# Kernel tuning notes

Hardware: AMD Instinct MI355X
Metric: run time of the kernel (lower is better)

The kernel has to match this reference:

```python
import jax, jax.numpy as jnp
import numpy as np

N = 4096
D = 256
H = 8
HD = D // H
EPS = 1e-5
NEG = -1e9


def layer_norm(x, g, b):
    mu = jnp.mean(x, axis=-1, keepdims=True)
    var = jnp.mean(jnp.square(x - mu), axis=-1, keepdims=True)
    return (x - mu) * jax.lax.rsqrt(var + EPS) * g + b


def setup_inputs() -> dict:
    key = jax.random.key(0)
    ks = jax.random.split(key, 12)
    s = 1.0 / np.sqrt(D)
    inp = {
        "x": jax.random.normal(ks[0], (N, D), dtype=jnp.float32),
        "adj": jax.random.randint(ks[1], (N, N), 0, 2, dtype=jnp.int32),
        "Wq": jax.random.uniform(ks[2], (D, D), jnp.float32, -s, s),
        "Wk": jax.random.uniform(ks[3], (D, D), jnp.float32, -s, s),
        "Wv": jax.random.uniform(ks[4], (D, D), jnp.float32, -s, s),
        "bq": jnp.zeros((D,), jnp.float32),
        "bk": jnp.zeros((D,), jnp.float32),
        "bv": jnp.zeros((D,), jnp.float32),
        "Wo": jax.random.uniform(ks[5], (D, D), jnp.float32, -s, s),
        "bo": jnp.zeros((D,), jnp.float32),
        "g1": jnp.ones((D,), jnp.float32),
        "beta1": jnp.zeros((D,), jnp.float32),
        "W1": jax.random.uniform(ks[6], (2 * D, D), jnp.float32, -s, s),
        "b1": jnp.zeros((2 * D,), jnp.float32),
        "W2": jax.random.uniform(ks[7], (D, 2 * D), jnp.float32, -1.0 / np.sqrt(2 * D), 1.0 / np.sqrt(2 * D)),
        "b2": jnp.zeros((D,), jnp.float32),
        "g2": jnp.ones((D,), jnp.float32),
        "beta2": jnp.zeros((D,), jnp.float32),
    }
    return inp


def reference(x, adj, Wq, Wk, Wv, bq, bk, bv, Wo, bo, g1, beta1, W1, b1, W2, b2, g2, beta2):
    n = adj.shape[0]
    # allowed = adj + I > 0 ; attention only over neighbors + self-loop
    allowed = (adj + jnp.eye(n, dtype=adj.dtype)) > 0  # (n, n) bool

    q = (x @ Wq.T + bq).reshape(n, H, HD)
    k = (x @ Wk.T + bk).reshape(n, H, HD)
    v = (x @ Wv.T + bv).reshape(n, H, HD)

    scale = 1.0 / np.sqrt(HD)
    scores = jnp.einsum('nhd,mhd->hnm', q, k) * scale  # (H, n, n)
    scores = jnp.where(allowed[None, :, :], scores, NEG)
    attn = jax.nn.softmax(scores, axis=-1)
    o = jnp.einsum('hnm,mhd->nhd', attn, v).reshape(n, D)
    h = o @ Wo.T + bo

    x = layer_norm(x + h, g1, beta1)
    ffn = jax.nn.relu(x @ W1.T + b1) @ W2.T + b2
    x = layer_norm(x + ffn, g2, beta2)
    return x
```

## Files before the change

### kernel.cpp

```cpp
#include <hip/hip_runtime.h>
#include <hip/hip_bf16.h>

typedef __attribute__((ext_vector_type(4))) float f32x4;
typedef __attribute__((ext_vector_type(8))) short s16x8;

#define NROWS 4096
#define DMODEL 256
#define NHEAD 8
#define HDIM 32
#define PSTRIDE 72
#define OSTRIDE 33
#define M2C 24.0f
#define NM (NROWS * DMODEL)
#define SH_S 268
#define SY_S 264
#define SR_S 520

__device__ __forceinline__ short bf16r(float f) {
    union { float f; unsigned u; } v; v.f = f;
    unsigned r = v.u + 0x7fffu + ((v.u >> 16) & 1u);
    return (short)(r >> 16);
}

__device__ __forceinline__ float fexp2(float x) {
    float r;
    asm("v_exp_f32 %0, %1" : "=v"(r) : "v"(x));
    return r;
}

__device__ __forceinline__ unsigned pk_bf16(float a, float b) {
#if __has_builtin(__builtin_amdgcn_cvt_pk_bf16_f32)
    typedef __bf16 bf2 __attribute__((ext_vector_type(2)));
    union { bf2 h; unsigned u; } c;
    c.h = __builtin_amdgcn_cvt_pk_bf16_f32(a, b);
    return c.u;
#else
    return (unsigned)(unsigned short)bf16r(a) | ((unsigned)(unsigned short)bf16r(b) << 16);
#endif
}

__device__ __forceinline__ s16x8 pack8(float4 a, float4 b) {
    s16x8 r;
    r[0] = bf16r(a.x); r[1] = bf16r(a.y); r[2] = bf16r(a.z); r[3] = bf16r(a.w);
    r[4] = bf16r(b.x); r[5] = bf16r(b.y); r[6] = bf16r(b.z); r[7] = bf16r(b.w);
    return r;
}

__global__ __launch_bounds__(256) void prep1_kernel(
        const int* __restrict__ adj, unsigned* __restrict__ mask,
        const float* __restrict__ Wo, const float* __restrict__ W1,
        const float* __restrict__ W2, short* __restrict__ Wb,
        const float* __restrict__ Wq, const float* __restrict__ Wk,
        const float* __restrict__ Wv, short* __restrict__ Wqkvb,
        const float* __restrict__ X, short* __restrict__ Xb) {
    const int b = blockIdx.x;
    const int tid = threadIdx.x;
    const int lane = tid & 63;
    if (b < 2048) {
        const int waveid = b * 4 + (tid >> 6);
        int4 av[8];
        int rows[8], segs[8];
#pragma unroll
        for (int i = 0; i < 8; ++i) {
            const int task = waveid + i * 8192;
            rows[i] = task >> 4; segs[i] = task & 15;
            av[i] = *(const int4*)(adj + (size_t)rows[i] * NROWS + segs[i] * 256 + lane * 4);
        }
#pragma unroll
        for (int i = 0; i < 8; ++i) {
            const int row = rows[i];
            const int c0 = segs[i] * 256 + lane * 4;
            unsigned nib = (unsigned)(av[i].x > 0 || c0 == row)
                         | ((unsigned)(av[i].y > 0 || c0 + 1 == row) << 1)
                         | ((unsigned)(av[i].z > 0 || c0 + 2 == row) << 2)
                         | ((unsigned)(av[i].w > 0 || c0 + 3 == row) << 3);
            unsigned v = nib << ((lane & 7) * 4);
            v |= __shfl_xor((int)v, 1, 64);
            v |= __shfl_xor((int)v, 2, 64);
            v |= __shfl_xor((int)v, 4, 64);
            if ((lane & 7) == 0)
                mask[row * 128 + segs[i] * 8 + (lane >> 3)] = v;
        }
    } else if (b < 2208) {
        int i = (b - 2048) * 2048 + tid * 8;
        const float* src; int off;
        if (i < 65536)       { src = Wo; off = i; }
        else if (i < 196608) { src = W1; off = i - 65536; }
        else                 { src = W2; off = i - 196608; }
        *(s16x8*)(Wb + i) = pack8(*(const float4*)(src + off), *(const float4*)(src + off + 4));
    } else if (b < 2304) {
        int i = (b - 2208) * 2048 + tid * 8;
        const float* src; int off;
        if (i < 65536)       { src = Wq; off = i; }
        else if (i < 131072) { src = Wk; off = i - 65536; }
        else                 { src = Wv; off = i - 131072; }
        *(s16x8*)(Wqkvb + i) = pack8(*(const float4*)(src + off), *(const float4*)(src + off + 4));
    } else {
        int i = (b - 2304) * 2048 + tid * 8;
        *(s16x8*)(Xb + i) = pack8(*(const float4*)(X + i), *(const float4*)(X + i + 4));
    }
}

__global__ __launch_bounds__(256) void prep2_kernel(
        const short* __restrict__ Xb, const short* __restrict__ Wqkvb,
        const float* __restrict__ bq, const float* __restrict__ bk,
        const float* __restrict__ bv,
        short* __restrict__ Qb, short* __restrict__ Kb,
        short* __restrict__ Vswz) {
    __shared__ short sT[64 * 72];
    const int b = blockIdx.x;
    const int tid = threadIdx.x;
    const int lane = tid & 63;
    const int wv = tid >> 6;
    const int quad = lane >> 4, col = lane & 15;
    const int bx = b & 63, by = b >> 6;
    const int o0 = by * 64;
    const int z = o0 >> 8;
    const float* bias = (z == 0) ? bq : (z == 1 ? bk : bv);
    const int ow0 = o0 & 255;
    const int n0 = bx * 64 + wv * 16;
    const float QSC = 0.25505653437397888f;

    f32x4 zero = {0.f, 0.f, 0.f, 0.f};
    f32x4 acc[4] = {zero, zero, zero, zero};
    const short* ap = Xb + (size_t)(n0 + col) * DMODEL + quad * 8;
#pragma unroll
    for (int k0 = 0; k0 < DMODEL; k0 += 32) {
        s16x8 af = *(const s16x8*)(ap + k0);
#pragma unroll
        for (int t = 0; t < 4; ++t) {
            s16x8 bf = *(const s16x8*)(Wqkvb + (size_t)(o0 + t * 16 + col) * DMODEL + quad * 8 + k0);
            acc[t] = __builtin_amdgcn_mfma_f32_16x16x32_bf16(af, bf, acc[t], 0, 0, 0);
        }
    }
    if (z != 2) {
#pragma unroll
        for (int t = 0; t < 4; ++t) {
            const int oo = ow0 + t * 16 + col;
            float bvv = bias[oo];
#pragma unroll
            for (int r = 0; r < 4; ++r) {
                int n = n0 + quad * 4 + r;
                float v = acc[t][r] + bvv;
                if (z == 0) Qb[(size_t)n * DMODEL + oo] = bf16r(v * QSC);
                else        Kb[(size_t)(oo >> 5) * NROWS * HDIM + (size_t)n * HDIM + (oo & 31)] = bf16r(v);
            }
        }
    } else {
#pragma unroll
        for (int t = 0; t < 4; ++t) {
            const int oot = t * 16 + col;
            float bvv = bias[ow0 + oot];
#pragma unroll
            for (int r = 0; r < 4; ++r) {
                int nn = wv * 16 + quad * 4 + r;
                sT[oot * 72 + nn] = bf16r(acc[t][r] + bvv);
            }
        }
        __syncthreads();
        const int f = tid >> 5;
        const int lh = f >> 2, hdh = (f >> 1) & 1, kh = f & 1;
        const int L0 = (tid & 31) * 2;
        const int hgl = (ow0 >> 5) + lh;
        short* dst = Vswz + (((size_t)(hgl * 64 + bx) * 4 + hdh * 2 + kh) * 512);
#pragma unroll
        for (int e = 0; e < 2; ++e) {
            int L = L0 + e;
            int hd_local = lh * 32 + hdh * 16 + (L & 15);
            int key_local = kh * 32 + ((L >> 4) * 8);
            s16x8 v = *(const s16x8*)&sT[hd_local * 72 + key_local];
            *(s16x8*)(dst + L * 8) = v;
        }
    }
}

__global__ __launch_bounds__(256) void attn_kernel(const short* __restrict__ Qb,
                                                   const short* __restrict__ Kb,
                                                   const short* __restrict__ Vswz,
                                                   const unsigned* __restrict__ mask,
                                                   short* __restrict__ Om) {
    __shared__ union {
        short sP[2][16 * PSTRIDE];
        float sO[HDIM][OSTRIDE];
    } u[4];
    __shared__ float sl[4][32];
    __shared__ __align__(16) unsigned lut2[32];

    const int tid = threadIdx.x;
    const int wv = tid >> 6, lane = tid & 63;
    const int quad = lane >> 4, col = lane & 15;
    const int h = blockIdx.x & 7;
    const int q0 = (blockIdx.x >> 3) * 32;
    const int kw = wv * 1024;

    if (tid < 32) {
        int i = tid >> 1;
        unsigned b0 = (tid & 1) ? ((i >> 2) & 1u) : (i & 1u);
        unsigned b1 = (tid & 1) ? ((i >> 3) & 1u) : ((i >> 1) & 1u);
        lut2[tid] = (b0 ? 0xFFFFu : 0u) | (b1 ? 0xFFFF0000u : 0u);
    }
    __syncthreads();

    s16x8 qf[2];
    qf[0] = *(const s16x8*)(Qb + (size_t)(q0 + col) * DMODEL + h * HDIM + quad * 8);
    qf[1] = *(const s16x8*)(Qb + (size_t)(q0 + 16 + col) * DMODEL + h * HDIM + quad * 8);

    const short* kp = Kb + (size_t)h * NROWS * HDIM + (size_t)(kw + col) * HDIM + quad * 8;
    const short* vbase = Vswz + ((size_t)(h * 64 + (kw >> 6)) * 4) * 512 + lane * 8;
    const unsigned* mp0 = mask + (size_t)(q0 + col) * 128 + (kw >> 5);
    const unsigned* mp1 = mp0 + 16 * 128;

    const short onev = (col == 0) ? (short)0x3F80 : (short)0;
    const s16x8 ones = {onev, onev, onev, onev, onev, onev, onev, onev};

    f32x4 zero = {0.f, 0.f, 0.f, 0.f};
    f32x4 acc[2][2] = {{zero, zero}, {zero, zero}};
    f32x4 lacc[2] = {zero, zero};
    const f32x4 cinit = {-M2C, -M2C, -M2C, -M2C};
    const int sh_lo = quad * 4, sh_hi = 16 + quad * 4;
    const char* lb = (const char*)lut2;

#pragma unroll 2
    for (int it = 0; it < 16; ++it) {
        const short* k = kp + it * 64 * HDIM;
        s16x8 kf0 = *(const s16x8*)(k);
        s16x8 kf1 = *(const s16x8*)(k + 16 * HDIM);
        s16x8 kf2 = *(const s16x8*)(k + 32 * HDIM);
        s16x8 kf3 = *(const s16x8*)(k + 48 * HDIM);
        uint2 w0 = *(const uint2*)(mp0 + it * 2);
        uint2 w1 = *(const uint2*)(mp1 + it * 2);
        const short* vb = vbase + it * 4 * 512;
        s16x8 vf00 = *(const s16x8*)(vb);
        s16x8 vf01 = *(const s16x8*)(vb + 512);
        s16x8 vf10 = *(const s16x8*)(vb + 1024);
        s16x8 vf11 = *(const s16x8*)(vb + 1536);

#pragma unroll
        for (int qs = 0; qs < 2; ++qs) {
            const unsigned wx = qs ? w1.x : w0.x;
            const unsigned wy = qs ? w1.y : w0.y;
            uint2 m0 = *(const uint2*)(lb + (((wx >> sh_lo) & 0xF) << 3));
            uint2 m1 = *(const uint2*)(lb + (((wx >> sh_hi) & 0xF) << 3));
            uint2 m2 = *(const uint2*)(lb + (((wy >> sh_lo) & 0xF) << 3));
            uint2 m3 = *(const uint2*)(lb + (((wy >> sh_hi) & 0xF) << 3));

            f32x4 st[4];
            st[0] = __builtin_amdgcn_mfma_f32_16x16x32_bf16(kf0, qf[qs], cinit, 0, 0, 0);
            st[1] = __builtin_amdgcn_mfma_f32_16x16x32_bf16(kf1, qf[qs], cinit, 0, 0, 0);
            st[2] = __builtin_amdgcn_mfma_f32_16x16x32_bf16(kf2, qf[qs], cinit, 0, 0, 0);
            st[3] = __builtin_amdgcn_mfma_f32_16x16x32_bf16(kf3, qf[qs], cinit, 0, 0, 0);

            short* pb = &u[wv].sP[qs][0];
            uint2 pr;
            pr.x = pk_bf16(fexp2(st[0][0]), fexp2(st[0][1])) & m0.x;
            pr.y = pk_bf16(fexp2(st[0][2]), fexp2(st[0][3])) & m0.y;
            *(uint2*)(pb + col * PSTRIDE + 0 * 16 + quad * 4) = pr;
            pr.x = pk_bf16(fexp2(st[1][0]), fexp2(st[1][1])) & m1.x;
            pr.y = pk_bf16(fexp2(st[1][2]), fexp2(st[1][3])) & m1.y;
            *(uint2*)(pb + col * PSTRIDE + 1 * 16 + quad * 4) = pr;
            pr.x = pk_bf16(fexp2(st[2][0]), fexp2(st[2][1])) & m2.x;
            pr.y = pk_bf16(fexp2(st[2][2]), fexp2(st[2][3])) & m2.y;
            *(uint2*)(pb + col * PSTRIDE + 2 * 16 + quad * 4) = pr;
            pr.x = pk_bf16(fexp2(st[3][0]), fexp2(st[3][1])) & m3.x;
            pr.y = pk_bf16(fexp2(st[3][2]), fexp2(st[3][3])) & m3.y;
            *(uint2*)(pb + col * PSTRIDE + 3 * 16 + quad * 4) = pr;

            s16x8 pb0 = *(const s16x8*)(pb + col * PSTRIDE + quad * 8);
            s16x8 pb1 = *(const s16x8*)(pb + col * PSTRIDE + 32 + quad * 8);

            acc[qs][0] = __builtin_amdgcn_mfma_f32_16x16x32_bf16(vf00, pb0, acc[qs][0], 0, 0, 0);
            acc[qs][0] = __builtin_amdgcn_mfma_f32_16x16x32_bf16(vf01, pb1, acc[qs][0], 0, 0, 0);
            acc[qs][1] = __builtin_amdgcn_mfma_f32_16x16x32_bf16(vf10, pb0, acc[qs][1], 0, 0, 0);
            acc[qs][1] = __builtin_amdgcn_mfma_f32_16x16x32_bf16(vf11, pb1, acc[qs][1], 0, 0, 0);
            lacc[qs] = __builtin_amdgcn_mfma_f32_16x16x32_bf16(ones, pb0, lacc[qs], 0, 0, 0);
            lacc[qs] = __builtin_amdgcn_mfma_f32_16x16x32_bf16(ones, pb1, lacc[qs], 0, 0, 0);
        }
    }

#pragma unroll
    for (int qs = 0; qs < 2; ++qs) {
        if (lane < 16) sl[wv][qs * 16 + col] = lacc[qs][0];
#pragma unroll
        for (int rr = 0; rr < 4; ++rr) {
            u[wv].sO[quad * 4 + rr][qs * 16 + col]      = acc[qs][0][rr];
            u[wv].sO[16 + quad * 4 + rr][qs * 16 + col] = acc[qs][1][rr];
        }
    }
    __syncthreads();

    const int q = tid >> 3, hd0 = (tid & 7) * 4;
    float l = sl[0][q] + sl[1][q] + sl[2][q] + sl[3][q];
    float inv = 1.f / l;
    float4 ov;
    ov.x = u[0].sO[hd0][q]     + u[1].sO[hd0][q]     + u[2].sO[hd0][q]     + u[3].sO[hd0][q];
    ov.y = u[0].sO[hd0 + 1][q] + u[1].sO[hd0 + 1][q] + u[2].sO[hd0 + 1][q] + u[3].sO[hd0 + 1][q];
    ov.z = u[0].sO[hd0 + 2][q] + u[1].sO[hd0 + 2][q] + u[2].sO[hd0 + 2][q] + u[3].sO[hd0 + 2][q];
    ov.w = u[0].sO[hd0 + 3][q] + u[1].sO[hd0 + 3][q] + u[2].sO[hd0 + 3][q] + u[3].sO[hd0 + 3][q];
    uint2 ob;
    ob.x = pk_bf16(ov.x * inv, ov.y * inv);
    ob.y = pk_bf16(ov.z * inv, ov.w * inv);
    *(uint2*)(Om + (size_t)(q0 + q) * DMODEL + h * HDIM + hd0) = ob;
}

__global__ __launch_bounds__(512) void mega_kernel(
        const short* __restrict__ Omb,
        const float* __restrict__ X,
        const short* __restrict__ Wob, const short* __restrict__ W1b,
        const short* __restrict__ W2b,
        const float* __restrict__ bo,
        const float* __restrict__ g1, const float* __restrict__ be1,
        const float* __restrict__ b1, const float* __restrict__ b2,
        const float* __restrict__ g2, const float* __restrict__ be2,
        float* __restrict__ out) {
    __shared__ short sR[16 * SR_S];
    __shared__ float sH[16 * SH_S];
    __shared__ short sY[16 * SY_S];

    const int tid = threadIdx.x;
    const int wv = tid >> 6, lane = tid & 63;
    const int quad = lane >> 4, col = lane & 15;
    const int n0 = blockIdx.x * 16;
    const int rr_ = tid >> 5, c8 = (tid & 31) * 8;
    const int n_ln = n0 + rr_;
    f32x4 zero = {0.f, 0.f, 0.f, 0.f};

    {
        const int o0 = wv * 32;
        f32x4 acc[2] = {zero, zero};
#pragma unroll
        for (int k0 = 0; k0 < DMODEL; k0 += 32) {
            s16x8 af = *(const s16x8*)(Omb + (size_t)(n0 + col) * DMODEL + k0 + quad * 8);
#pragma unroll
            for (int t = 0; t < 2; ++t) {
                s16x8 bf = *(const s16x8*)(Wob + (size_t)(o0 + t * 16 + col) * DMODEL + k0 + quad * 8);
                acc[t] = __builtin_amdgcn_mfma_f32_16x16x32_bf16(af, bf, acc[t], 0, 0, 0);
            }
        }
#pragma unroll
        for (int t = 0; t < 2; ++t) {
            int o = o0 + t * 16 + col;
            float bv = bo[o];
#pragma unroll
            for (int r = 0; r < 4; ++r)
                sH[(quad * 4 + r) * SH_S + o] = acc[t][r] + bv;
        }
    }
    __syncthreads();

    float y1v[8];
    {
        const float* xp = X + (size_t)n_ln * DMODEL + c8;
        float v[8];
        float s = 0.f;
#pragma unroll
        for (int j = 0; j < 2; ++j) {
            float4 xv = ((const float4*)xp)[j];
            float4 hv = *(const float4*)&sH[rr_ * SH_S + c8 + j * 4];
            v[j * 4 + 0] = xv.x + hv.x; v[j * 4 + 1] = xv.y + hv.y;
            v[j * 4 + 2] = xv.z + hv.z; v[j * 4 + 3] = xv.w + hv.w;
            s += v[j * 4] + v[j * 4 + 1] + v[j * 4 + 2] + v[j * 4 + 3];
        }
#pragma unroll
        for (int m = 1; m < 32; m <<= 1) s += __shfl_xor(s, m, 64);
        float mean = s * (1.f / 256.f);
        float q = 0.f;
#pragma unroll
        for (int i = 0; i < 8; ++i) { v[i] -= mean; q += v[i] * v[i]; }
#pragma unroll
        for (int m = 1; m < 32; m <<= 1) q += __shfl_xor(q, m, 64);
        float rstd = rsqrtf(q * (1.f / 256.f) + 1e-5f);
        const float* gp = g1 + c8;
        const float* bp = be1 + c8;
        s16x8 w;
#pragma unroll
        for (int j = 0; j < 2; ++j) {
            float4 gv = ((const float4*)gp)[j];
            float4 bev = ((const float4*)bp)[j];
            float a0 = v[j * 4 + 0] * rstd * gv.x + bev.x;
            float a1 = v[j * 4 + 1] * rstd * gv.y + bev.y;
            float a2 = v[j * 4 + 2] * rstd * gv.z + bev.z;
            float a3 = v[j * 4 + 3] * rstd * gv.w + bev.w;
            y1v[j * 4 + 0] = a0; y1v[j * 4 + 1] = a1;
            y1v[j * 4 + 2] = a2; y1v[j * 4 + 3] = a3;
            *((unsigned*)&w + j * 2 + 0) = pk_bf16(a0, a1);
            *((unsigned*)&w + j * 2 + 1) = pk_bf16(a2, a3);
        }
        *(s16x8*)&sY[rr_ * SY_S + c8] = w;
    }
    __syncthreads();

    {
        const int o0 = wv * 64;
        f32x4 acc[4] = {zero, zero, zero, zero};
#pragma unroll
        for (int k0 = 0; k0 < DMODEL; k0 += 32) {
            s16x8 af = *(const s16x8*)&sY[col * SY_S + k0 + quad * 8];
#pragma unroll
            for (int t = 0; t < 4; ++t) {
                s16x8 bf = *(const s16x8*)(W1b + (size_t)(o0 + t * 16 + col) * DMODEL + k0 + quad * 8);
                acc[t] = __builtin_amdgcn_mfma_f32_16x16x32_bf16(af, bf, acc[t], 0, 0, 0);
            }
        }
#pragma unroll
        for (int t = 0; t < 4; ++t) {
            int o = o0 + t * 16 + col;
            float bv = b1[o];
#pragma unroll
            for (int r = 0; r < 4; ++r)
                sR[(quad * 4 + r) * SR_S + o] = bf16r(fmaxf(acc[t][r] + bv, 0.f));
        }
    }
    __syncthreads();

    {
        const int o0 = wv * 32;
        f32x4 acc[2] = {zero, zero};
#pragma unroll
        for (int k0 = 0; k0 < 512; k0 += 32) {
            s16x8 af = *(const s16x8*)&sR[col * SR_S + k0 + quad * 8];
#pragma unroll
            for (int t = 0; t < 2; ++t) {
                s16x8 bf = *(const s16x8*)(W2b + (size_t)(o0 + t * 16 + col) * 512 + k0 + quad * 8);
                acc[t] = __builtin_amdgcn_mfma_f32_16x16x32_bf16(af, bf, acc[t], 0, 0, 0);
            }
        }
#pragma unroll
        for (int t = 0; t < 2; ++t) {
            int o = o0 + t * 16 + col;
            float bv = b2[o];
#pragma unroll
            for (int r = 0; r < 4; ++r)
                sH[(quad * 4 + r) * SH_S + o] = acc[t][r] + bv;
        }
    }
    __syncthreads();

    {
        float v[8];
        float s = 0.f;
#pragma unroll
        for (int j = 0; j < 2; ++j) {
            float4 hv = *(const float4*)&sH[rr_ * SH_S + c8 + j * 4];
            v[j * 4 + 0] = y1v[j * 4 + 0] + hv.x; v[j * 4 + 1] = y1v[j * 4 + 1] + hv.y;
            v[j * 4 + 2] = y1v[j * 4 + 2] + hv.z; v[j * 4 + 3] = y1v[j * 4 + 3] + hv.w;
            s += v[j * 4] + v[j * 4 + 1] + v[j * 4 + 2] + v[j * 4 + 3];
        }
#pragma unroll
        for (int m = 1; m < 32; m <<= 1) s += __shfl_xor(s, m, 64);
        float mean = s * (1.f / 256.f);
        float q = 0.f;
#pragma unroll
        for (int i = 0; i < 8; ++i) { v[i] -= mean; q += v[i] * v[i]; }
#pragma unroll
        for (int m = 1; m < 32; m <<= 1) q += __shfl_xor(q, m, 64);
        float rstd = rsqrtf(q * (1.f / 256.f) + 1e-5f);
        const float* gp = g2 + c8;
        const float* bp = be2 + c8;
        float* op = out + (size_t)n_ln * DMODEL + c8;
#pragma unroll
        for (int j = 0; j < 2; ++j) {
            float4 gv = ((const float4*)gp)[j];
            float4 bev = ((const float4*)bp)[j];
            float4 y;
            y.x = v[j * 4 + 0] * rstd * gv.x + bev.x;
            y.y = v[j * 4 + 1] * rstd * gv.y + bev.y;
            y.z = v[j * 4 + 2] * rstd * gv.z + bev.z;
            y.w = v[j * 4 + 3] * rstd * gv.w + bev.w;
            ((float4*)op)[j] = y;
        }
    }
}

extern "C" void kernel_launch(void* const* d_in, const int* in_sizes, int n_in,
                              void* d_out, int out_size, void* d_ws, size_t ws_size,
                              hipStream_t stream) {
    const float* x   = (const float*)d_in[0];
    const int*   adj = (const int*)d_in[1];
    const float* Wq  = (const float*)d_in[2];
    const float* Wk  = (const float*)d_in[3];
    const float* Wv  = (const float*)d_in[4];
    const float* bq  = (const float*)d_in[5];
    const float* bk  = (const float*)d_in[6];
    const float* bv  = (const float*)d_in[7];
    const float* Wo  = (const float*)d_in[8];
    const float* bo  = (const float*)d_in[9];
    const float* g1  = (const float*)d_in[10];
    const float* be1 = (const float*)d_in[11];
    const float* W1  = (const float*)d_in[12];
    const float* b1  = (const float*)d_in[13];
    const float* W2  = (const float*)d_in[14];
    const float* b2  = (const float*)d_in[15];
    const float* g2  = (const float*)d_in[16];
    const float* be2 = (const float*)d_in[17];
    float* out = (float*)d_out;

    char* p = (char*)d_ws;
    unsigned* mask = (unsigned*)p; p += (size_t)NROWS * 128 * 4;
    short* Wb    = (short*)p;      p += (size_t)327680 * 2;
    short* Wqkvb = (short*)p;      p += (size_t)196608 * 2;
    short* Xb    = (short*)p;      p += (size_t)NM * 2;
    short* Qb    = (short*)p;      p += (size_t)NM * 2;
    short* Kb    = (short*)p;      p += (size_t)NM * 2;
    short* Vswz  = (short*)p;      p += (size_t)NM * 2;
    short* Omb   = (short*)p;      p += (size_t)NM * 2;

    prep1_kernel<<<dim3(2816), dim3(256), 0, stream>>>(
        adj, mask, Wo, W1, W2, Wb, Wq, Wk, Wv, Wqkvb, x, Xb);
    prep2_kernel<<<dim3(768), dim3(256), 0, stream>>>(
        Xb, Wqkvb, bq, bk, bv, Qb, Kb, Vswz);
    attn_kernel<<<dim3(1024), dim3(256), 0, stream>>>(Qb, Kb, Vswz, mask, Omb);
    mega_kernel<<<dim3(256), dim3(512), 0, stream>>>(
        Omb, x, Wb, Wb + 65536, Wb + 196608,
        bo, g1, be1, b1, b2, g2, be2, out);
}
```

Baseline: 212.2 us.

## Keep softmax probabilities in registers by permuting the V key layout

```diff
diff --git a/kernel.cpp b/kernel.cpp
--- a/kernel.cpp
+++ b/kernel.cpp
@@ -8,7 +8,6 @@
 #define DMODEL 256
 #define NHEAD 8
 #define HDIM 32
-#define PSTRIDE 72
 #define OSTRIDE 33
 #define M2C 24.0f
 #define NM (NROWS * DMODEL)
@@ -167,9 +166,11 @@
         for (int e = 0; e < 2; ++e) {
             int L = L0 + e;
             int hd_local = lh * 32 + hdh * 16 + (L & 15);
-            int key_local = kh * 32 + ((L >> 4) * 8);
-            s16x8 v = *(const s16x8*)&sT[hd_local * 72 + key_local];
-            *(s16x8*)(dst + L * 8) = v;
+            int base = kh * 32 + (L >> 4) * 4;
+            uint2 lo = *(const uint2*)&sT[hd_local * 72 + base];
+            uint2 hi = *(const uint2*)&sT[hd_local * 72 + base + 16];
+            *(uint2*)(dst + L * 8) = lo;
+            *(uint2*)(dst + L * 8 + 4) = hi;
         }
     }
 }
@@ -179,10 +180,7 @@
                                                    const short* __restrict__ Vswz,
                                                    const unsigned* __restrict__ mask,
                                                    short* __restrict__ Om) {
-    __shared__ union {
-        short sP[2][16 * PSTRIDE];
-        float sO[HDIM][OSTRIDE];
-    } u[4];
+    __shared__ float sO[4][HDIM][OSTRIDE];
     __shared__ float sl[4][32];
     __shared__ __align__(16) unsigned lut2[32];
 
@@ -250,30 +248,22 @@
             st[2] = __builtin_amdgcn_mfma_f32_16x16x32_bf16(kf2, qf[qs], cinit, 0, 0, 0);
             st[3] = __builtin_amdgcn_mfma_f32_16x16x32_bf16(kf3, qf[qs], cinit, 0, 0, 0);
 
-            short* pb = &u[wv].sP[qs][0];
-            uint2 pr;
-            pr.x = pk_bf16(fexp2(st[0][0]), fexp2(st[0][1])) & m0.x;
-            pr.y = pk_bf16(fexp2(st[0][2]), fexp2(st[0][3])) & m0.y;
-            *(uint2*)(pb + col * PSTRIDE + 0 * 16 + quad * 4) = pr;
-            pr.x = pk_bf16(fexp2(st[1][0]), fexp2(st[1][1])) & m1.x;
-            pr.y = pk_bf16(fexp2(st[1][2]), fexp2(st[1][3])) & m1.y;
-            *(uint2*)(pb + col * PSTRIDE + 1 * 16 + quad * 4) = pr;
-            pr.x = pk_bf16(fexp2(st[2][0]), fexp2(st[2][1])) & m2.x;
-            pr.y = pk_bf16(fexp2(st[2][2]), fexp2(st[2][3])) & m2.y;
-            *(uint2*)(pb + col * PSTRIDE + 2 * 16 + quad * 4) = pr;
-            pr.x = pk_bf16(fexp2(st[3][0]), fexp2(st[3][1])) & m3.x;
-            pr.y = pk_bf16(fexp2(st[3][2]), fexp2(st[3][3])) & m3.y;
-            *(uint2*)(pb + col * PSTRIDE + 3 * 16 + quad * 4) = pr;
-
-            s16x8 pb0 = *(const s16x8*)(pb + col * PSTRIDE + quad * 8);
-            s16x8 pb1 = *(const s16x8*)(pb + col * PSTRIDE + 32 + quad * 8);
-
-            acc[qs][0] = __builtin_amdgcn_mfma_f32_16x16x32_bf16(vf00, pb0, acc[qs][0], 0, 0, 0);
-            acc[qs][0] = __builtin_amdgcn_mfma_f32_16x16x32_bf16(vf01, pb1, acc[qs][0], 0, 0, 0);
-            acc[qs][1] = __builtin_amdgcn_mfma_f32_16x16x32_bf16(vf10, pb0, acc[qs][1], 0, 0, 0);
-            acc[qs][1] = __builtin_amdgcn_mfma_f32_16x16x32_bf16(vf11, pb1, acc[qs][1], 0, 0, 0);
-            lacc[qs] = __builtin_amdgcn_mfma_f32_16x16x32_bf16(ones, pb0, lacc[qs], 0, 0, 0);
-            lacc[qs] = __builtin_amdgcn_mfma_f32_16x16x32_bf16(ones, pb1, lacc[qs], 0, 0, 0);
+            union { unsigned u[4]; s16x8 v; } P0, P1;
+            P0.u[0] = pk_bf16(fexp2(st[0][0]), fexp2(st[0][1])) & m0.x;
+            P0.u[1] = pk_bf16(fexp2(st[0][2]), fexp2(st[0][3])) & m0.y;
+            P0.u[2] = pk_bf16(fexp2(st[1][0]), fexp2(st[1][1])) & m1.x;
+            P0.u[3] = pk_bf16(fexp2(st[1][2]), fexp2(st[1][3])) & m1.y;
+            P1.u[0] = pk_bf16(fexp2(st[2][0]), fexp2(st[2][1])) & m2.x;
+            P1.u[1] = pk_bf16(fexp2(st[2][2]), fexp2(st[2][3])) & m2.y;
+            P1.u[2] = pk_bf16(fexp2(st[3][0]), fexp2(st[3][1])) & m3.x;
+            P1.u[3] = pk_bf16(fexp2(st[3][2]), fexp2(st[3][3])) & m3.y;
+
+            acc[qs][0] = __builtin_amdgcn_mfma_f32_16x16x32_bf16(vf00, P0.v, acc[qs][0], 0, 0, 0);
+            acc[qs][0] = __builtin_amdgcn_mfma_f32_16x16x32_bf16(vf01, P1.v, acc[qs][0], 0, 0, 0);
+            acc[qs][1] = __builtin_amdgcn_mfma_f32_16x16x32_bf16(vf10, P0.v, acc[qs][1], 0, 0, 0);
+            acc[qs][1] = __builtin_amdgcn_mfma_f32_16x16x32_bf16(vf11, P1.v, acc[qs][1], 0, 0, 0);
+            lacc[qs] = __builtin_amdgcn_mfma_f32_16x16x32_bf16(ones, P0.v, lacc[qs], 0, 0, 0);
+            lacc[qs] = __builtin_amdgcn_mfma_f32_16x16x32_bf16(ones, P1.v, lacc[qs], 0, 0, 0);
         }
     }
 
@@ -282,8 +272,8 @@
         if (lane < 16) sl[wv][qs * 16 + col] = lacc[qs][0];
 #pragma unroll
         for (int rr = 0; rr < 4; ++rr) {
-            u[wv].sO[quad * 4 + rr][qs * 16 + col]      = acc[qs][0][rr];
-            u[wv].sO[16 + quad * 4 + rr][qs * 16 + col] = acc[qs][1][rr];
+            sO[wv][quad * 4 + rr][qs * 16 + col]      = acc[qs][0][rr];
+            sO[wv][16 + quad * 4 + rr][qs * 16 + col] = acc[qs][1][rr];
         }
     }
     __syncthreads();
@@ -292,10 +282,10 @@
     float l = sl[0][q] + sl[1][q] + sl[2][q] + sl[3][q];
     float inv = 1.f / l;
     float4 ov;
-    ov.x = u[0].sO[hd0][q]     + u[1].sO[hd0][q]     + u[2].sO[hd0][q]     + u[3].sO[hd0][q];
-    ov.y = u[0].sO[hd0 + 1][q] + u[1].sO[hd0 + 1][q] + u[2].sO[hd0 + 1][q] + u[3].sO[hd0 + 1][q];
-    ov.z = u[0].sO[hd0 + 2][q] + u[1].sO[hd0 + 2][q] + u[2].sO[hd0 + 2][q] + u[3].sO[hd0 + 2][q];
-    ov.w = u[0].sO[hd0 + 3][q] + u[1].sO[hd0 + 3][q] + u[2].sO[hd0 + 3][q] + u[3].sO[hd0 + 3][q];
+    ov.x = sO[0][hd0][q]     + sO[1][hd0][q]     + sO[2][hd0][q]     + sO[3][hd0][q];
+    ov.y = sO[0][hd0 + 1][q] + sO[1][hd0 + 1][q] + sO[2][hd0 + 1][q] + sO[3][hd0 + 1][q];
+    ov.z = sO[0][hd0 + 2][q] + sO[1][hd0 + 2][q] + sO[2][hd0 + 2][q] + sO[3][hd0 + 2][q];
+    ov.w = sO[0][hd0 + 3][q] + sO[1][hd0 + 3][q] + sO[2][hd0 + 3][q] + sO[3][hd0 + 3][q];
     uint2 ob;
     ob.x = pk_bf16(ov.x * inv, ov.y * inv);
     ob.y = pk_bf16(ov.z * inv, ov.w * inv);
```

Result: no change. 210.5 us (-0.8%).
